# Kernel tuning notes

Hardware: AMD Instinct MI355X
Metric: run time of the kernel (lower is better)

The kernel has to match this reference:

```python
import jax, jax.numpy as jnp
import numpy as np

WINDOW = 20  # window_size from init

def setup_inputs() -> dict:
    key = jax.random.key(0)
    ks = jax.random.split(key, 8)
    B, K, L, H = 8, 64, 1024, 256
    FFN = 3 * H * 4  # input_dim*ffn_ratio
    cand_span_reps = jax.random.normal(ks[0], (B, K, H), dtype=jnp.float32)
    token_reps = jax.random.normal(ks[1], (B, L, H), dtype=jnp.float32)
    W1 = jax.random.normal(ks[2], (3 * H, FFN), dtype=jnp.float32) * (1.0 / np.sqrt(3 * H))
    b1 = jnp.zeros((FFN,), dtype=jnp.float32)
    W2 = jax.random.normal(ks[3], (FFN, H), dtype=jnp.float32) * (1.0 / np.sqrt(FFN))
    b2 = jnp.zeros((H,), dtype=jnp.float32)
    cand_span_ids = jnp.sort(jax.random.randint(ks[4], (B, K, 2), 0, L), axis=-1)
    token_masks = jnp.ones((B, L), dtype=bool)
    return {"cand_span_reps": cand_span_reps, "token_reps": token_reps,
            "W1": W1, "b1": b1, "W2": W2, "b2": b2,
            "cand_span_ids": cand_span_ids, "token_masks": token_masks}

def _span_window_max(token_reps, span_ids, token_masks, window):
    # token_reps: [B,L,H]; span_ids: [B,K,2]; token_masks: [B,L]
    L = token_reps.shape[1]
    seq = jnp.arange(L)[None, None, :]                      # [1,1,L]
    start = span_ids[:, :, 0][:, :, None]                   # [B,K,1]
    end = span_ids[:, :, 1][:, :, None]                     # [B,K,1]
    mask = (((seq >= start - window) & (seq < start)) |
            ((seq > end) & (seq <= end + window)))
    mask = mask & token_masks[:, None, :]                   # [B,K,L]
    # masked max over L -> [B,K,H]
    filled = jnp.where(mask[..., None], token_reps[:, None, :, :], -jnp.inf)
    return jnp.max(filled, axis=2)

def reference(cand_span_reps, token_reps, W1, b1, W2, b2, cand_span_ids, token_masks):
    B, K, H = cand_span_reps.shape
    # Per-span pooled window context [B,K,H]. The pairwise context over the
    # UNION of head & tail windows equals the elementwise max of the two
    # per-span window maxes (max over A|B == max(max A, max B)).
    ctx = _span_window_max(token_reps, cand_span_ids, token_masks, WINDOW)
    context_reps = jnp.maximum(ctx[:, :, None, :], ctx[:, None, :, :])   # [B,K,K,H]
    head_reps = jnp.broadcast_to(cand_span_reps[:, :, None, :], (B, K, K, H))
    tail_reps = jnp.broadcast_to(cand_span_reps[:, None, :, :], (B, K, K, H))
    rel = jnp.concatenate([head_reps, tail_reps, context_reps], axis=-1)  # [B,K,K,3H]
    h = jax.nn.relu(jnp.einsum('bijd,df->bijf', rel, W1) + b1)
    out = jnp.einsum('bijf,fh->bijh', h, W2) + b2
    return out.reshape(B, K * K, H)
```

## Files before the change

kernel.cpp:

```cpp
#include <hip/hip_runtime.h>
#include <hip/hip_bf16.h>
#include <cstdint>
#include <cstddef>


typedef __attribute__((ext_vector_type(8))) short short8;
typedef __attribute__((ext_vector_type(4))) float f32x4;
typedef __attribute__((ext_vector_type(2))) unsigned int u32x2;

#define B_DIM 8
#define K_DIM 64
#define H_DIM 256
#define L_DIM 1024
#define FFN_DIM 3072
#define WINDOW 20

__device__ __forceinline__ unsigned short f2b(float f) {
  unsigned int u = __float_as_uint(f);
  unsigned int r = (u + 0x7FFFu + ((u >> 16) & 1u)) >> 16;
  return (unsigned short)r;
}
__device__ __forceinline__ float b2f(unsigned short h) {
  return __uint_as_float(((unsigned int)h) << 16);
}
__device__ __forceinline__ f32x4 zero4() {
  f32x4 z = {0.f, 0.f, 0.f, 0.f};
  return z;
}
__device__ __forceinline__ void gload_lds16(const void* g, void* l) {
  __builtin_amdgcn_global_load_lds(
      (const __attribute__((address_space(1))) void*)g,
      (__attribute__((address_space(3))) void*)l, 16, 0, 0);
}
__device__ __forceinline__ unsigned int cvt_pk_bf16(float lo, float hi) {
  unsigned int r;
  asm("v_cvt_pk_bf16_f32 %0, %1, %2" : "=v"(r) : "v"(lo), "v"(hi));
  return r;
}


__global__ void cvt_bf16_kernel(const float* __restrict__ in,
                                unsigned short* __restrict__ out, int n) {
  int i = blockIdx.x * blockDim.x + threadIdx.x;
  if (i < n) out[i] = f2b(in[i]);
}

__global__ void transpose_cvt_kernel(const float* __restrict__ in,
                                     unsigned short* __restrict__ out,
                                     int R, int C) {
  __shared__ float t[64][65];
  int c0 = blockIdx.x * 64, r0 = blockIdx.y * 64;
  int tr = threadIdx.x >> 6, tc = threadIdx.x & 63;
  for (int rr = tr; rr < 64; rr += 4)
    t[rr][tc] = in[(size_t)(r0 + rr) * C + (c0 + tc)];
  __syncthreads();
  for (int cc = tr; cc < 64; cc += 4)
    out[(size_t)(c0 + cc) * R + (r0 + tc)] = f2b(t[tc][cc]);
}

__global__ void ctx_kernel(const float* __restrict__ token,
                           const int* __restrict__ ids,
                           unsigned short* __restrict__ ctx) {
  int bk = blockIdx.x;
  int b = bk >> 6;
  int h = threadIdx.x;
  int s = ids[bk * 2 + 0];
  int e = ids[bk * 2 + 1];
  const float* tb = token + ((size_t)b * L_DIM) * H_DIM + h;
  float m = -INFINITY;
  int lo = s - WINDOW; if (lo < 0) lo = 0;
  for (int l2 = lo; l2 < s; ++l2) m = fmaxf(m, tb[(size_t)l2 * H_DIM]);
  int hi = e + WINDOW; if (hi > L_DIM - 1) hi = L_DIM - 1;
  for (int l2 = e + 1; l2 <= hi; ++l2) m = fmaxf(m, tb[(size_t)l2 * H_DIM]);
  ctx[(size_t)bk * H_DIM + h] = f2b(m);
}

__global__ __launch_bounds__(256) void at_gemm_kernel(
    const unsigned short* __restrict__ candb,
    const unsigned short* __restrict__ w1abt,
    const float* __restrict__ b1, float* __restrict__ AT) {
  int n0 = blockIdx.x * 64;
  int r0 = blockIdx.y * 64;
  __shared__ __align__(16) unsigned short A[64 * 256];
  int w = threadIdx.x >> 6, l = threadIdx.x & 63;
  int l15 = l & 15, l4 = l >> 4;
  {
    int row = w * 16 + l15;
    const short8* src = (const short8*)(candb + (size_t)(r0 + row) * H_DIM);
    #pragma unroll
    for (int t = 0; t < 8; ++t) {
      int u = l4 + 4 * t;
      short8 v = src[u];
      *(short8*)(A + row * 256 + ((u ^ (row & 7)) * 8)) = v;
    }
  }
  __syncthreads();
  f32x4 acc[4] = {zero4(), zero4(), zero4(), zero4()};
  int n = n0 + 16 * w + l15;
  const unsigned short* bp = w1abt + (size_t)n * H_DIM + l4 * 8;
  #pragma unroll
  for (int kk = 0; kk < 8; ++kk) {
    short8 bfrag = *(const short8*)(bp + kk * 32);
    #pragma unroll
    for (int rf = 0; rf < 4; ++rf) {
      int row = rf * 16 + l15;
      int u = kk * 4 + l4;
      short8 afrag = *(const short8*)(A + row * 256 + ((u ^ (row & 7)) * 8));
      acc[rf] = __builtin_amdgcn_mfma_f32_16x16x32_bf16(afrag, bfrag, acc[rf], 0, 0, 0);
    }
  }
  float bias = (n < FFN_DIM) ? b1[n] : 0.0f;
  #pragma unroll
  for (int rf = 0; rf < 4; ++rf) {
    #pragma unroll
    for (int qq = 0; qq < 4; ++qq) {
      int row = r0 + rf * 16 + l4 * 4 + qq;
      AT[(size_t)row * (2 * FFN_DIM) + n] = acc[rf][qq] + bias;
    }
  }
}

__global__ __launch_bounds__(512, 4) void fused_kernel(
    const unsigned short* __restrict__ ctx,
    const unsigned short* __restrict__ w1ct,
    const unsigned short* __restrict__ w2t,
    const float* __restrict__ AT,
    const float* __restrict__ b2,
    float* __restrict__ out) {
  int blk = blockIdx.x;
  blk = (blk & 7) * 64 + (blk >> 3);
  int b = blk >> 6, i = blk & 63;

  __shared__ __align__(16) char W1s[2 * 16384];
  __shared__ __align__(16) char W2s[2 * 16384];
  __shared__ __align__(16) char HcS[4096];

  int tid = threadIdx.x;
  int w = tid >> 6, l = tid & 63;
  int l15 = l & 15, l4 = l >> 4;
  int wl = l15 & 7;
  int s3 = (l15 >> 1) & 3;

  if (w < 4) {
    int wf = w & 1, wj2 = w >> 1;
    int jloc = 32 * wj2 + l15;

    short8 bfr[8][2];
    {
      const unsigned short* cb = ctx + ((size_t)b * K_DIM) * H_DIM;
      const unsigned short* ci = cb + (size_t)i * H_DIM;
      #pragma unroll
      for (int kk = 0; kk < 8; ++kk) {
        int hoff = kk * 32 + l4 * 8;
        short8 vi = *(const short8*)(ci + hoff);
        #pragma unroll
        for (int jb = 0; jb < 2; ++jb) {
          short8 vj = *(const short8*)(cb + (size_t)(jloc + jb * 16) * H_DIM + hoff);
          short8 vm;
          #pragma unroll
          for (int e = 0; e < 8; ++e) {
            float fa = b2f((unsigned short)vi[e]);
            float fb = b2f((unsigned short)vj[e]);
            vm[e] = (fa >= fb) ? vi[e] : vj[e];
          }
          bfr[kk][jb] = vm;
        }
      }
    }

    int tid_p = (w << 6) | l;
    int fr = tid_p >> 5, u32i = tid_p & 31;
    int offW1 = fr * 512 + (((u32i & 24) | ((u32i & 7) ^ (fr & 7))) << 4);
    auto stageW1 = [&](int c, int buf) {
      const char* g = (const char*)w1ct + (size_t)c * 16384 + offW1;
      char* d = &W1s[buf * 16384 + tid_p * 16];
      gload_lds16(g, d);
      gload_lds16(g + 4096, d + 4096);
      gload_lds16(g + 8192, d + 8192);
      gload_lds16(g + 12288, d + 12288);
    };

    int baseA = (16 * wf + l15) * 512;
    int offAe = (l4 ^ wl) << 4;
    int offAo = ((4 + l4) ^ wl) << 4;
    int uW = 2 * wf + (l4 >> 1);
    int offHw = jloc * 64 + ((uW ^ s3) << 4) + ((l4 & 1) << 3);

    const float* avp = AT + (size_t)(b * K_DIM + i) * (2 * FFN_DIM) + 16 * wf + 4 * l4;
    const float* tvp = AT + (size_t)(b * K_DIM + jloc) * (2 * FFN_DIM) + FFN_DIM + 16 * wf + 4 * l4;

    stageW1(0, 0);
    __builtin_amdgcn_sched_barrier(0);
    asm volatile("s_waitcnt vmcnt(0)" ::: "memory");
    __builtin_amdgcn_sched_barrier(0);
    __builtin_amdgcn_s_barrier();
    __builtin_amdgcn_sched_barrier(0);

    for (int c = 0; c < 96; ++c) {
      f32x4 av  = *(const f32x4*)(avp + c * 32);
      f32x4 tv0 = *(const f32x4*)(tvp + c * 32);
      f32x4 tv1 = *(const f32x4*)(tvp + 16 * (2 * FFN_DIM) + c * 32);
      __builtin_amdgcn_sched_barrier(0);
      stageW1(c < 95 ? c + 1 : 95, (c + 1) & 1);
      __builtin_amdgcn_sched_barrier(0);

      const char* w1p = &W1s[(c & 1) * 16384 + baseA];
      f32x4 acc1[2] = {zero4(), zero4()};
      __builtin_amdgcn_s_setprio(1);
      #pragma unroll
      for (int m = 0; m < 4; ++m) {
        short8 afe = *(const short8*)(w1p + m * 128 + offAe);
        acc1[0] = __builtin_amdgcn_mfma_f32_16x16x32_bf16(afe, bfr[2 * m][0], acc1[0], 0, 0, 0);
        acc1[1] = __builtin_amdgcn_mfma_f32_16x16x32_bf16(afe, bfr[2 * m][1], acc1[1], 0, 0, 0);
        short8 afo = *(const short8*)(w1p + m * 128 + offAo);
        acc1[0] = __builtin_amdgcn_mfma_f32_16x16x32_bf16(afo, bfr[2 * m + 1][0], acc1[0], 0, 0, 0);
        acc1[1] = __builtin_amdgcn_mfma_f32_16x16x32_bf16(afo, bfr[2 * m + 1][1], acc1[1], 0, 0, 0);
      }
      __builtin_amdgcn_s_setprio(0);

      {
        float v0 = fmaxf(acc1[0][0] + av[0] + tv0[0], 0.0f);
        float v1 = fmaxf(acc1[0][1] + av[1] + tv0[1], 0.0f);
        float v2 = fmaxf(acc1[0][2] + av[2] + tv0[2], 0.0f);
        float v3 = fmaxf(acc1[0][3] + av[3] + tv0[3], 0.0f);
        u32x2 pk;
        pk.x = cvt_pk_bf16(v0, v1);
        pk.y = cvt_pk_bf16(v2, v3);
        *(u32x2*)(HcS + offHw) = pk;
      }
      {
        float v0 = fmaxf(acc1[1][0] + av[0] + tv1[0], 0.0f);
        float v1 = fmaxf(acc1[1][1] + av[1] + tv1[1], 0.0f);
        float v2 = fmaxf(acc1[1][2] + av[2] + tv1[2], 0.0f);
        float v3 = fmaxf(acc1[1][3] + av[3] + tv1[3], 0.0f);
        u32x2 pk;
        pk.x = cvt_pk_bf16(v0, v1);
        pk.y = cvt_pk_bf16(v2, v3);
        *(u32x2*)(HcS + offHw + 1024) = pk;
      }
      __builtin_amdgcn_sched_barrier(0);
      asm volatile("s_waitcnt lgkmcnt(0)" ::: "memory");
      __builtin_amdgcn_sched_barrier(0);
      __builtin_amdgcn_s_barrier();
      __builtin_amdgcn_sched_barrier(0);
      asm volatile("s_waitcnt vmcnt(0)" ::: "memory");
      __builtin_amdgcn_sched_barrier(0);
      __builtin_amdgcn_s_barrier();
      __builtin_amdgcn_sched_barrier(0);
    }
  } else {
    int ch = w - 4;
    int tid_c = (ch << 6) | l;
    int h2 = tid_c >> 2, u2 = tid_c & 3;
    int offW2 = h2 * 6144 + ((u2 ^ ((h2 >> 1) & 3)) << 4);
    auto stageW2 = [&](int c, int buf) {
      const char* g = (const char*)w2t + (size_t)c * 64 + offW2;
      char* d = &W2s[buf * 16384 + tid_c * 16];
      gload_lds16(g, d);
      gload_lds16(g + 1 * 393216, d + 4096);
      gload_lds16(g + 2 * 393216, d + 8192);
      gload_lds16(g + 3 * 393216, d + 12288);
    };
    int baseW2 = ch * 4096 + l15 * 64 + ((l4 ^ s3) << 4);
    int baseHr = l15 * 64 + ((l4 ^ s3) << 4);

    f32x4 accO[4][4];
    #pragma unroll
    for (int cf = 0; cf < 4; ++cf)
      #pragma unroll
      for (int jt = 0; jt < 4; ++jt) accO[cf][jt] = zero4();

    stageW2(0, 0);
    __builtin_amdgcn_sched_barrier(0);
    asm volatile("s_waitcnt vmcnt(0)" ::: "memory");
    __builtin_amdgcn_sched_barrier(0);
    __builtin_amdgcn_s_barrier();
    __builtin_amdgcn_sched_barrier(0);

    for (int c = 0; c < 96; ++c) {
      stageW2(c < 95 ? c + 1 : 95, (c + 1) & 1);
      __builtin_amdgcn_sched_barrier(0);
      asm volatile("s_waitcnt vmcnt(4)" ::: "memory");
      __builtin_amdgcn_sched_barrier(0);
      __builtin_amdgcn_s_barrier();
      __builtin_amdgcn_sched_barrier(0);

      const char* w2p = &W2s[(c & 1) * 16384];
      short8 wfr[4], hbv[4];
      #pragma unroll
      for (int cf = 0; cf < 4; ++cf)
        wfr[cf] = *(const short8*)(w2p + baseW2 + cf * 1024);
      #pragma unroll
      for (int jt = 0; jt < 4; ++jt)
        hbv[jt] = *(const short8*)(HcS + baseHr + jt * 1024);
      __builtin_amdgcn_s_setprio(1);
      #pragma unroll
      for (int cf = 0; cf < 4; ++cf)
        #pragma unroll
        for (int jt = 0; jt < 4; ++jt)
          accO[cf][jt] = __builtin_amdgcn_mfma_f32_16x16x32_bf16(wfr[cf], hbv[jt], accO[cf][jt], 0, 0, 0);
      __builtin_amdgcn_s_setprio(0);

      __builtin_amdgcn_sched_barrier(0);
      asm volatile("s_waitcnt lgkmcnt(0)" ::: "memory");
      __builtin_amdgcn_sched_barrier(0);
      __builtin_amdgcn_s_barrier();
      __builtin_amdgcn_sched_barrier(0);
    }

    f32x4 bv[4];
    #pragma unroll
    for (int cf = 0; cf < 4; ++cf)
      bv[cf] = *(const f32x4*)(b2 + 64 * ch + cf * 16 + 4 * l4);
    #pragma unroll
    for (int jt = 0; jt < 4; ++jt) {
      int j = jt * 16 + l15;
      float* row = out + ((size_t)b * (K_DIM * K_DIM) + (size_t)i * K_DIM + j) * H_DIM;
      #pragma unroll
      for (int cf = 0; cf < 4; ++cf) {
        f32x4 v = accO[cf][jt] + bv[cf];
        *(f32x4*)(row + 64 * ch + cf * 16 + 4 * l4) = v;
      }
    }
  }
}


extern "C" void kernel_launch(void* const* d_in, const int* in_sizes, int n_in,
                              void* d_out, int out_size, void* d_ws, size_t ws_size,
                              hipStream_t stream) {
  const float* cand  = (const float*)d_in[0];
  const float* token = (const float*)d_in[1];
  const float* W1    = (const float*)d_in[2];
  const float* b1    = (const float*)d_in[3];
  const float* W2    = (const float*)d_in[4];
  const float* b2    = (const float*)d_in[5];
  const int*   ids   = (const int*)d_in[6];
  float* out = (float*)d_out;

  char* ws = (char*)d_ws;
  unsigned short* ctx   = (unsigned short*)(ws);
  unsigned short* candb = (unsigned short*)(ws + 262144);
  unsigned short* w1abt = (unsigned short*)(ws + 524288);
  unsigned short* w1ct  = (unsigned short*)(ws + 3670016);
  unsigned short* w2t   = (unsigned short*)(ws + 5242880);
  float*          AT    = (float*)(ws + 6815744);

  hipLaunchKernelGGL(cvt_bf16_kernel, dim3(512), dim3(256), 0, stream,
                     cand, candb, B_DIM * K_DIM * H_DIM);
  hipLaunchKernelGGL(transpose_cvt_kernel, dim3(48, 4), dim3(256), 0, stream,
                     W1, w1abt, 256, FFN_DIM);
  hipLaunchKernelGGL(transpose_cvt_kernel, dim3(48, 4), dim3(256), 0, stream,
                     W1 + (size_t)256 * FFN_DIM, w1abt + (size_t)FFN_DIM * 256, 256, FFN_DIM);
  hipLaunchKernelGGL(transpose_cvt_kernel, dim3(48, 4), dim3(256), 0, stream,
                     W1 + (size_t)512 * FFN_DIM, w1ct, 256, FFN_DIM);
  hipLaunchKernelGGL(transpose_cvt_kernel, dim3(4, 48), dim3(256), 0, stream,
                     W2, w2t, FFN_DIM, 256);
  hipLaunchKernelGGL(ctx_kernel, dim3(512), dim3(256), 0, stream, token, ids, ctx);
  hipLaunchKernelGGL(at_gemm_kernel, dim3(96, 8), dim3(256), 0, stream,
                     candb, w1abt, b1, AT);
  hipLaunchKernelGGL(fused_kernel, dim3(512), dim3(512), 0, stream,
                     ctx, w1ct, w2t, AT, b2, out);
}
```

Measured before the change: 189.5 us.

## Double-buffer hidden tile to overlap FFN stages with one barrier per chunk

Gives the hidden-activation LDS tile two buffers so the producer waves (first GEMM plus ReLU) can compute chunk c while the consumer waves (second GEMM) work on chunk c-1. The loop runs one extra step as a skew, and two barriers per iteration become one. This removes the serialisation where producer waves idled while consumers read the single hidden buffer. The cost is 4 KB more LDS, which may affect occupancy, plus a one-stage pipeline prologue and epilogue.

```diff
diff --git a/kernel.cpp b/kernel.cpp
--- a/kernel.cpp
+++ b/kernel.cpp
@@ -133,7 +133,7 @@
 
   __shared__ __align__(16) char W1s[2 * 16384];
   __shared__ __align__(16) char W2s[2 * 16384];
-  __shared__ __align__(16) char HcS[4096];
+  __shared__ __align__(16) char HcS[2 * 4096];
 
   int tid = threadIdx.x;
   int w = tid >> 6, l = tid & 63;
@@ -196,54 +196,57 @@
     __builtin_amdgcn_s_barrier();
     __builtin_amdgcn_sched_barrier(0);
 
-    for (int c = 0; c < 96; ++c) {
-      f32x4 av  = *(const f32x4*)(avp + c * 32);
-      f32x4 tv0 = *(const f32x4*)(tvp + c * 32);
-      f32x4 tv1 = *(const f32x4*)(tvp + 16 * (2 * FFN_DIM) + c * 32);
-      __builtin_amdgcn_sched_barrier(0);
-      stageW1(c < 95 ? c + 1 : 95, (c + 1) & 1);
-      __builtin_amdgcn_sched_barrier(0);
-
-      const char* w1p = &W1s[(c & 1) * 16384 + baseA];
-      f32x4 acc1[2] = {zero4(), zero4()};
-      __builtin_amdgcn_s_setprio(1);
-      #pragma unroll
-      for (int m = 0; m < 4; ++m) {
-        short8 afe = *(const short8*)(w1p + m * 128 + offAe);
-        acc1[0] = __builtin_amdgcn_mfma_f32_16x16x32_bf16(afe, bfr[2 * m][0], acc1[0], 0, 0, 0);
-        acc1[1] = __builtin_amdgcn_mfma_f32_16x16x32_bf16(afe, bfr[2 * m][1], acc1[1], 0, 0, 0);
-        short8 afo = *(const short8*)(w1p + m * 128 + offAo);
-        acc1[0] = __builtin_amdgcn_mfma_f32_16x16x32_bf16(afo, bfr[2 * m + 1][0], acc1[0], 0, 0, 0);
-        acc1[1] = __builtin_amdgcn_mfma_f32_16x16x32_bf16(afo, bfr[2 * m + 1][1], acc1[1], 0, 0, 0);
-      }
-      __builtin_amdgcn_s_setprio(0);
-
-      {
-        float v0 = fmaxf(acc1[0][0] + av[0] + tv0[0], 0.0f);
-        float v1 = fmaxf(acc1[0][1] + av[1] + tv0[1], 0.0f);
-        float v2 = fmaxf(acc1[0][2] + av[2] + tv0[2], 0.0f);
-        float v3 = fmaxf(acc1[0][3] + av[3] + tv0[3], 0.0f);
-        u32x2 pk;
-        pk.x = cvt_pk_bf16(v0, v1);
-        pk.y = cvt_pk_bf16(v2, v3);
-        *(u32x2*)(HcS + offHw) = pk;
-      }
-      {
-        float v0 = fmaxf(acc1[1][0] + av[0] + tv1[0], 0.0f);
-        float v1 = fmaxf(acc1[1][1] + av[1] + tv1[1], 0.0f);
-        float v2 = fmaxf(acc1[1][2] + av[2] + tv1[2], 0.0f);
-        float v3 = fmaxf(acc1[1][3] + av[3] + tv1[3], 0.0f);
-        u32x2 pk;
-        pk.x = cvt_pk_bf16(v0, v1);
-        pk.y = cvt_pk_bf16(v2, v3);
-        *(u32x2*)(HcS + offHw + 1024) = pk;
-      }
-      __builtin_amdgcn_sched_barrier(0);
-      asm volatile("s_waitcnt lgkmcnt(0)" ::: "memory");
-      __builtin_amdgcn_sched_barrier(0);
-      __builtin_amdgcn_s_barrier();
-      __builtin_amdgcn_sched_barrier(0);
-      asm volatile("s_waitcnt vmcnt(0)" ::: "memory");
+    for (int c = 0; c <= 96; ++c) {
+      f32x4 av = zero4(), tv0 = zero4(), tv1 = zero4();
+      if (c < 96) {
+        av  = *(const f32x4*)(avp + c * 32);
+        tv0 = *(const f32x4*)(tvp + c * 32);
+        tv1 = *(const f32x4*)(tvp + 16 * (2 * FFN_DIM) + c * 32);
+      }
+      __builtin_amdgcn_sched_barrier(0);
+      if (c < 95) stageW1(c + 1, (c + 1) & 1);
+      __builtin_amdgcn_sched_barrier(0);
+
+      if (c < 96) {
+        const char* w1p = &W1s[(c & 1) * 16384 + baseA];
+        f32x4 acc1[2] = {zero4(), zero4()};
+        __builtin_amdgcn_s_setprio(1);
+        #pragma unroll
+        for (int m = 0; m < 4; ++m) {
+          short8 afe = *(const short8*)(w1p + m * 128 + offAe);
+          acc1[0] = __builtin_amdgcn_mfma_f32_16x16x32_bf16(afe, bfr[2 * m][0], acc1[0], 0, 0, 0);
+          acc1[1] = __builtin_amdgcn_mfma_f32_16x16x32_bf16(afe, bfr[2 * m][1], acc1[1], 0, 0, 0);
+          short8 afo = *(const short8*)(w1p + m * 128 + offAo);
+          acc1[0] = __builtin_amdgcn_mfma_f32_16x16x32_bf16(afo, bfr[2 * m + 1][0], acc1[0], 0, 0, 0);
+          acc1[1] = __builtin_amdgcn_mfma_f32_16x16x32_bf16(afo, bfr[2 * m + 1][1], acc1[1], 0, 0, 0);
+        }
+        __builtin_amdgcn_s_setprio(0);
+
+        char* hw = &HcS[(c & 1) * 4096];
+        {
+          float v0 = fmaxf(acc1[0][0] + av[0] + tv0[0], 0.0f);
+          float v1 = fmaxf(acc1[0][1] + av[1] + tv0[1], 0.0f);
+          float v2 = fmaxf(acc1[0][2] + av[2] + tv0[2], 0.0f);
+          float v3 = fmaxf(acc1[0][3] + av[3] + tv0[3], 0.0f);
+          u32x2 pk;
+          pk.x = cvt_pk_bf16(v0, v1);
+          pk.y = cvt_pk_bf16(v2, v3);
+          *(u32x2*)(hw + offHw) = pk;
+        }
+        {
+          float v0 = fmaxf(acc1[1][0] + av[0] + tv1[0], 0.0f);
+          float v1 = fmaxf(acc1[1][1] + av[1] + tv1[1], 0.0f);
+          float v2 = fmaxf(acc1[1][2] + av[2] + tv1[2], 0.0f);
+          float v3 = fmaxf(acc1[1][3] + av[3] + tv1[3], 0.0f);
+          u32x2 pk;
+          pk.x = cvt_pk_bf16(v0, v1);
+          pk.y = cvt_pk_bf16(v2, v3);
+          *(u32x2*)(hw + offHw + 1024) = pk;
+        }
+      }
+
+      __builtin_amdgcn_sched_barrier(0);
+      asm volatile("s_waitcnt vmcnt(0) lgkmcnt(0)" ::: "memory");
       __builtin_amdgcn_sched_barrier(0);
       __builtin_amdgcn_s_barrier();
       __builtin_amdgcn_sched_barrier(0);
@@ -270,39 +273,34 @@
       #pragma unroll
       for (int jt = 0; jt < 4; ++jt) accO[cf][jt] = zero4();
 
-    stageW2(0, 0);
-    __builtin_amdgcn_sched_barrier(0);
-    asm volatile("s_waitcnt vmcnt(0)" ::: "memory");
-    __builtin_amdgcn_sched_barrier(0);
     __builtin_amdgcn_s_barrier();
     __builtin_amdgcn_sched_barrier(0);
 
-    for (int c = 0; c < 96; ++c) {
-      stageW2(c < 95 ? c + 1 : 95, (c + 1) & 1);
-      __builtin_amdgcn_sched_barrier(0);
-      asm volatile("s_waitcnt vmcnt(4)" ::: "memory");
-      __builtin_amdgcn_sched_barrier(0);
-      __builtin_amdgcn_s_barrier();
-      __builtin_amdgcn_sched_barrier(0);
-
-      const char* w2p = &W2s[(c & 1) * 16384];
-      short8 wfr[4], hbv[4];
-      #pragma unroll
-      for (int cf = 0; cf < 4; ++cf)
-        wfr[cf] = *(const short8*)(w2p + baseW2 + cf * 1024);
-      #pragma unroll
-      for (int jt = 0; jt < 4; ++jt)
-        hbv[jt] = *(const short8*)(HcS + baseHr + jt * 1024);
-      __builtin_amdgcn_s_setprio(1);
-      #pragma unroll
-      for (int cf = 0; cf < 4; ++cf)
+    for (int c = 0; c <= 96; ++c) {
+      if (c < 96) stageW2(c, c & 1);
+      __builtin_amdgcn_sched_barrier(0);
+
+      if (c > 0) {
+        const char* w2p = &W2s[((c - 1) & 1) * 16384];
+        const char* hcp = &HcS[((c - 1) & 1) * 4096];
+        short8 wfr[4], hbv[4];
+        #pragma unroll
+        for (int cf = 0; cf < 4; ++cf)
+          wfr[cf] = *(const short8*)(w2p + baseW2 + cf * 1024);
         #pragma unroll
         for (int jt = 0; jt < 4; ++jt)
-          accO[cf][jt] = __builtin_amdgcn_mfma_f32_16x16x32_bf16(wfr[cf], hbv[jt], accO[cf][jt], 0, 0, 0);
-      __builtin_amdgcn_s_setprio(0);
-
-      __builtin_amdgcn_sched_barrier(0);
-      asm volatile("s_waitcnt lgkmcnt(0)" ::: "memory");
+          hbv[jt] = *(const short8*)(hcp + baseHr + jt * 1024);
+        __builtin_amdgcn_s_setprio(1);
+        #pragma unroll
+        for (int cf = 0; cf < 4; ++cf)
+          #pragma unroll
+          for (int jt = 0; jt < 4; ++jt)
+            accO[cf][jt] = __builtin_amdgcn_mfma_f32_16x16x32_bf16(wfr[cf], hbv[jt], accO[cf][jt], 0, 0, 0);
+        __builtin_amdgcn_s_setprio(0);
+      }
+
+      __builtin_amdgcn_sched_barrier(0);
+      asm volatile("s_waitcnt vmcnt(0) lgkmcnt(0)" ::: "memory");
       __builtin_amdgcn_sched_barrier(0);
       __builtin_amdgcn_s_barrier();
       __builtin_amdgcn_sched_barrier(0);
```

Result: faster. 185.6 us (-2.0%).
